# Performance work log

Hardware: AMD Instinct MI355X
Metric: run time of the kernel (lower is better)

Reference implementation:

```python
import jax, jax.numpy as jnp
import numpy as np

NUM_GRAPHS = 128
NODES_PER_GRAPH = 512
N_NODES = NUM_GRAPHS * NODES_PER_GRAPH
N_EDGES = 524288
IN_DIM = 128
HID = 128
OUT_DIM = 10
N_LAYERS = 3
POOL_RATIO = 0.5  # TopKPooling default ratio


def setup_inputs() -> dict:
    key = jax.random.key(0)
    ks = jax.random.split(key, 16)
    x = jax.random.normal(ks[0], (N_NODES, IN_DIM), dtype=jnp.float32)
    edge_index = jax.random.randint(ks[1], (2, N_EDGES), 0, N_NODES, dtype=jnp.int64)
    batch = jnp.repeat(jnp.arange(NUM_GRAPHS, dtype=jnp.int64), NODES_PER_GRAPH)
    s = 0.05
    return {
        "x": x,
        "edge_index": edge_index,
        "batch": batch,
        "emb_W": jax.random.normal(ks[2], (IN_DIM, HID), dtype=jnp.float32) * s,
        "emb_b": jnp.zeros((HID,), dtype=jnp.float32),
        "gcn_W": jax.random.normal(ks[3], (N_LAYERS, HID, HID), dtype=jnp.float32) * s,
        "gcn_b": jnp.zeros((N_LAYERS, HID), dtype=jnp.float32),
        "pool_p": jax.random.normal(ks[4], (HID,), dtype=jnp.float32),
        "fc1_W": jax.random.normal(ks[5], (HID, 128), dtype=jnp.float32) * s,
        "fc1_b": jnp.zeros((128,), dtype=jnp.float32),
        "fc2_W": jax.random.normal(ks[6], (128, 64), dtype=jnp.float32) * s,
        "fc2_b": jnp.zeros((64,), dtype=jnp.float32),
        "fc3_W": jax.random.normal(ks[7], (64, OUT_DIM), dtype=jnp.float32) * s,
        "fc3_b": jnp.zeros((OUT_DIM,), dtype=jnp.float32),
    }


def reference(x, edge_index, batch, emb_W, emb_b, gcn_W, gcn_b, pool_p,
              fc1_W, fc1_b, fc2_W, fc2_b, fc3_W, fc3_b):
    n = x.shape[0]
    # embedding
    h = x @ emb_W + emb_b
    # GCNConv normalization (PyG semantics): add self loops, deg from target scatter
    loop = jnp.arange(n, dtype=edge_index.dtype)
    src = jnp.concatenate([edge_index[0], loop])
    dst = jnp.concatenate([edge_index[1], loop])
    deg = jax.ops.segment_sum(jnp.ones_like(src, dtype=h.dtype), dst, num_segments=n)
    dinv = jnp.where(deg > 0, jax.lax.rsqrt(jnp.maximum(deg, 1e-12)), 0.0)
    norm = dinv[src] * dinv[dst]  # [E+n]
    for l in range(gcn_W.shape[0]):
        hw = h @ gcn_W[l]                                   # [n, HID]
        msg = hw[src] * norm[:, None]                        # gather + scale
        h = jax.nn.relu(jax.ops.segment_sum(msg, dst, num_segments=n) + gcn_b[l])
    # TopKPooling (ratio=0.5, tanh nonlinearity), uniform graphs -> reshape + top_k
    npg = n // NUM_GRAPHS
    k = int(np.ceil(POOL_RATIO * npg))
    score = (h @ pool_p) / jnp.linalg.norm(pool_p)           # [n]
    score_g = score.reshape(NUM_GRAPHS, npg)
    topv, topi = jax.lax.top_k(score_g, k)                   # [G, k]
    h_g = h.reshape(NUM_GRAPHS, npg, -1)
    h_sel = jnp.take_along_axis(h_g, topi[:, :, None], axis=1) * jnp.tanh(topv)[:, :, None]
    pooled = h_sel.mean(axis=1)                              # global_mean_pool -> [G, HID]
    # MLP head (dropout is identity in eval)
    z = jax.nn.relu(pooled @ fc1_W + fc1_b)
    z = jax.nn.relu(z @ fc2_W + fc2_b)
    return z @ fc3_W + fc3_b
```

## Files before the change

kernel.cpp:

```cpp
#include <hip/hip_runtime.h>
#include <hip/hip_bf16.h>
#include <math.h>


#define SLOTS 48

static __device__ __forceinline__ float4 f4add(float4 a, float4 b) {
    return make_float4(a.x + b.x, a.y + b.y, a.z + b.z, a.w + b.w);
}
static __device__ __forceinline__ float4 f4fma(float s, float4 a, float4 acc) {
    return make_float4(fmaf(s, a.x, acc.x), fmaf(s, a.y, acc.y),
                       fmaf(s, a.z, acc.z), fmaf(s, a.w, acc.w));
}

__global__ __launch_bounds__(256) void build_graph_fold(
    const int* __restrict__ src, const int* __restrict__ dst,
    int* __restrict__ cnt, int* __restrict__ csr_pad, int E, int EB,
    const float* __restrict__ embW, const float* __restrict__ embb,
    const float* __restrict__ W0, float* __restrict__ W01,
    float* __restrict__ b01, float* __restrict__ zrowA,
    float* __restrict__ zrowB)
{
    const int b = blockIdx.x;
    if (b < EB) {
        int e = b * 256 + threadIdx.x;
        if (e < E) {
            int d = dst[e];
            int r = atomicAdd(&cnt[d], 1);
            if (r < SLOTS) csr_pad[d * SLOTS + r] = src[e];
        }
        return;
    }
    __shared__ float rs[128];
    __shared__ float part[256];
    const int r = b - EB;
    const int t = threadIdx.x;
    if (r == 0 && t < 128) { zrowA[t] = 0.f; zrowB[t] = 0.f; }
    const int c = t & 127, q = t >> 7;
    if (t < 128) rs[t] = (r < 128) ? embW[r * 128 + t] : embb[t];
    __syncthreads();
    float s = 0.f;
    const int k0 = q * 64;
#pragma unroll 8
    for (int k = k0; k < k0 + 64; k++) s = fmaf(rs[k], W0[k * 128 + c], s);
    part[t] = s;
    __syncthreads();
    if (q == 0) {
        float v = part[c] + part[c + 128];
        if (r < 128) W01[r * 128 + c] = v;
        else         b01[c] = v;
    }
}

#define ASTRIDE 129
#define WSTRIDE 140
__global__ __launch_bounds__(256) void gemm128(
    const float* __restrict__ A, const float* __restrict__ W,
    const float* __restrict__ bias, const int* __restrict__ rowdeg,
    float* __restrict__ out, int n)
{
    __shared__ float As[32 * ASTRIDE];
    __shared__ float Ws[32 * WSTRIDE];
    const int tid  = threadIdx.x;
    const int rb   = blockIdx.x * 128;
    const int tc   = tid & 15;
    const int tr   = tid >> 4;
    const int colg = tc * 8;
    const int cswz = colg + ((colg >> 5) << 2);
    const int rowg = tr * 8;

    const int a_kq = tid & 7;
    const int a_m  = tid >> 3;
    const int w_c  = (tid & 31) * 4;
    const int w_cs = w_c + ((w_c >> 5) << 2);
    const int w_k  = tid >> 5;

    float acc[8][8];
#pragma unroll
    for (int i = 0; i < 8; i++)
#pragma unroll
        for (int j = 0; j < 8; j++) acc[i][j] = 0.f;

    float4 areg[4], wreg[4];
#pragma unroll
    for (int t = 0; t < 4; t++)
        areg[t] = *(const float4*)&A[(size_t)(rb + t * 32 + a_m) * 128 + a_kq * 4];
#pragma unroll
    for (int t = 0; t < 4; t++)
        wreg[t] = *(const float4*)&W[(size_t)(t * 8 + w_k) * 128 + w_c];

#pragma unroll 1
    for (int k0 = 0; k0 < 128; k0 += 32) {
#pragma unroll
        for (int t = 0; t < 4; t++) {
            const int m = t * 32 + a_m;
            const float4 av = areg[t];
            As[(a_kq * 4 + 0) * ASTRIDE + m] = av.x;
            As[(a_kq * 4 + 1) * ASTRIDE + m] = av.y;
            As[(a_kq * 4 + 2) * ASTRIDE + m] = av.z;
            As[(a_kq * 4 + 3) * ASTRIDE + m] = av.w;
        }
#pragma unroll
        for (int t = 0; t < 4; t++)
            *(float4*)&Ws[(t * 8 + w_k) * WSTRIDE + w_cs] = wreg[t];
        __syncthreads();
        if (k0 < 96) {
#pragma unroll
            for (int t = 0; t < 4; t++)
                areg[t] = *(const float4*)&A[(size_t)(rb + t * 32 + a_m) * 128 + k0 + 32 + a_kq * 4];
#pragma unroll
            for (int t = 0; t < 4; t++)
                wreg[t] = *(const float4*)&W[(size_t)(k0 + 32 + t * 8 + w_k) * 128 + w_c];
        }
#pragma unroll 8
        for (int kk = 0; kk < 32; kk++) {
            float4 a0 = *(const float4*)&As[kk * ASTRIDE + rowg];
            float4 a1 = *(const float4*)&As[kk * ASTRIDE + rowg + 4];
            float4 b0 = *(const float4*)&Ws[kk * WSTRIDE + cswz];
            float4 b1 = *(const float4*)&Ws[kk * WSTRIDE + cswz + 4];
            float av[8] = {a0.x, a0.y, a0.z, a0.w, a1.x, a1.y, a1.z, a1.w};
            float bv[8] = {b0.x, b0.y, b0.z, b0.w, b1.x, b1.y, b1.z, b1.w};
#pragma unroll
            for (int i = 0; i < 8; i++)
#pragma unroll
                for (int j = 0; j < 8; j++) acc[i][j] = fmaf(av[i], bv[j], acc[i][j]);
        }
        __syncthreads();
    }

    float4 bb0 = make_float4(0.f, 0.f, 0.f, 0.f), bb1 = bb0;
    if (bias) {
        bb0 = *(const float4*)&bias[colg];
        bb1 = *(const float4*)&bias[colg + 4];
    }
#pragma unroll
    for (int i = 0; i < 8; i++) {
        const int row  = rb + rowg + i;
        const float sc = rowdeg ? rsqrtf((float)(rowdeg[row] + 1)) : 1.f;
        float4 o0, o1;
        o0.x = (acc[i][0] + bb0.x) * sc;  o0.y = (acc[i][1] + bb0.y) * sc;
        o0.z = (acc[i][2] + bb0.z) * sc;  o0.w = (acc[i][3] + bb0.w) * sc;
        o1.x = (acc[i][4] + bb1.x) * sc;  o1.y = (acc[i][5] + bb1.y) * sc;
        o1.z = (acc[i][6] + bb1.z) * sc;  o1.w = (acc[i][7] + bb1.w) * sc;
        *(float4*)&out[(size_t)row * 128 + colg]     = o0;
        *(float4*)&out[(size_t)row * 128 + colg + 4] = o1;
    }
}

__global__ __launch_bounds__(256) void agg_gemm(
    const float* __restrict__ hs_in, const int* __restrict__ csr_pad,
    const int* __restrict__ cnt, const float* __restrict__ aggb,
    const float* __restrict__ W, float* __restrict__ hs_out, int n)
{
    __shared__ int   s_idx[128 * 17];
    __shared__ float s_dinv[128];
    __shared__ int   s_deg[128];
    __shared__ float As[32 * ASTRIDE];
    __shared__ float Ws[32 * WSTRIDE];

    const int tid = threadIdx.x;
    const int rb  = blockIdx.x * 128;
    const float4* __restrict__ hv = (const float4*)hs_in;

    if (tid < 128) {
        int d = cnt[rb + tid];
        s_deg[tid]  = d;
        s_dinv[tid] = rsqrtf((float)(d + 1));
    }
    {
        const int m    = tid >> 1;
        const int hf   = (tid & 1) * 8;
        const int node = rb + m;
        const int4 cA = *(const int4*)&csr_pad[node * SLOTS + hf];
        const int4 cB = *(const int4*)&csr_pad[node * SLOTS + hf + 4];
        const int  d  = cnt[node];
        int* row = &s_idx[m * 17 + hf];
        row[0] = (hf + 0 < d) ? cA.x : n;
        row[1] = (hf + 1 < d) ? cA.y : n;
        row[2] = (hf + 2 < d) ? cA.z : n;
        row[3] = (hf + 3 < d) ? cA.w : n;
        row[4] = (hf + 4 < d) ? cB.x : n;
        row[5] = (hf + 5 < d) ? cB.y : n;
        row[6] = (hf + 6 < d) ? cB.z : n;
        row[7] = (hf + 7 < d) ? cB.w : n;
    }
    __syncthreads();

    const int tc   = tid & 15;
    const int tr   = tid >> 4;
    const int colg = tc * 8;
    const int cswz = colg + ((colg >> 5) << 2);
    const int rowg = tr * 8;
    const int w_c  = (tid & 31) * 4;
    const int w_cs = w_c + ((w_c >> 5) << 2);
    const int w_k  = tid >> 5;
    const int ln = tid & 7;
    const int nd = tid >> 3;

    float acc[8][8];
#pragma unroll
    for (int i = 0; i < 8; i++)
#pragma unroll
        for (int j = 0; j < 8; j++) acc[i][j] = 0.f;

#pragma unroll 1
    for (int p = 0; p < 4; p++) {
        float4 wreg[4];
#pragma unroll
        for (int t = 0; t < 4; t++)
            wreg[t] = *(const float4*)&W[(size_t)(p * 32 + t * 8 + w_k) * 128 + w_c];

        const int fo = p * 8 + ln;
        const float4 bb = *(const float4*)&aggb[p * 32 + ln * 4];
#pragma unroll 1
        for (int ps = 0; ps < 4; ps++) {
            const int m    = ps * 32 + nd;
            const int node = rb + m;
            const int* rowI = &s_idx[m * 17];
            float4 self = hv[(size_t)node * 32 + fo];
            float4 r[16];
#pragma unroll
            for (int j = 0; j < 16; j++)
                r[j] = hv[(size_t)rowI[j] * 32 + fo];
            asm volatile("" ::: "memory");
            float4 a0 = self;
            float4 a1 = make_float4(0.f, 0.f, 0.f, 0.f);
            float4 a2 = a1, a3 = a1;
#pragma unroll
            for (int j = 0; j < 16; j += 4) {
                a0 = f4add(a0, r[j + 0]);
                a1 = f4add(a1, r[j + 1]);
                a2 = f4add(a2, r[j + 2]);
                a3 = f4add(a3, r[j + 3]);
            }
            const int d    = s_deg[m];
            const int dcap = d < SLOTS ? d : SLOTS;
            for (int j = 16; j < dcap; j++)
                a1 = f4add(a1, hv[(size_t)csr_pad[node * SLOTS + j] * 32 + fo]);
            float4 s = f4add(f4add(a0, a1), f4add(a2, a3));
            const float dv = s_dinv[m];
            float4 o;
            o.x = fmaxf(fmaf(s.x, dv, bb.x), 0.f);
            o.y = fmaxf(fmaf(s.y, dv, bb.y), 0.f);
            o.z = fmaxf(fmaf(s.z, dv, bb.z), 0.f);
            o.w = fmaxf(fmaf(s.w, dv, bb.w), 0.f);
            const int kb = ln * 4;
            As[(kb + 0) * ASTRIDE + m] = o.x;
            As[(kb + 1) * ASTRIDE + m] = o.y;
            As[(kb + 2) * ASTRIDE + m] = o.z;
            As[(kb + 3) * ASTRIDE + m] = o.w;
        }
#pragma unroll
        for (int t = 0; t < 4; t++)
            *(float4*)&Ws[(t * 8 + w_k) * WSTRIDE + w_cs] = wreg[t];
        __syncthreads();

#pragma unroll 8
        for (int kk = 0; kk < 32; kk++) {
            float4 a0 = *(const float4*)&As[kk * ASTRIDE + rowg];
            float4 a1 = *(const float4*)&As[kk * ASTRIDE + rowg + 4];
            float4 b0 = *(const float4*)&Ws[kk * WSTRIDE + cswz];
            float4 b1 = *(const float4*)&Ws[kk * WSTRIDE + cswz + 4];
            float av[8] = {a0.x, a0.y, a0.z, a0.w, a1.x, a1.y, a1.z, a1.w};
            float bv[8] = {b0.x, b0.y, b0.z, b0.w, b1.x, b1.y, b1.z, b1.w};
#pragma unroll
            for (int i = 0; i < 8; i++)
#pragma unroll
                for (int j = 0; j < 8; j++) acc[i][j] = fmaf(av[i], bv[j], acc[i][j]);
        }
        __syncthreads();
    }

#pragma unroll
    for (int i = 0; i < 8; i++) {
        const int row  = rb + rowg + i;
        const float sc = s_dinv[rowg + i];
        float4 o0, o1;
        o0.x = acc[i][0] * sc;  o0.y = acc[i][1] * sc;
        o0.z = acc[i][2] * sc;  o0.w = acc[i][3] * sc;
        o1.x = acc[i][4] * sc;  o1.y = acc[i][5] * sc;
        o1.z = acc[i][6] * sc;  o1.w = acc[i][7] * sc;
        *(float4*)&hs_out[(size_t)row * 128 + colg]     = o0;
        *(float4*)&hs_out[(size_t)row * 128 + colg + 4] = o1;
    }
}

__global__ __launch_bounds__(256) void aggregate(
    const float* __restrict__ hs, const int* __restrict__ csr_pad,
    const int* __restrict__ cnt, const float* __restrict__ bias,
    float* __restrict__ hout,
    const float* __restrict__ pool_p, float* __restrict__ scores, int n)
{
    const int grp  = threadIdx.x >> 5;
    const int lane = threadIdx.x & 31;
    const int node = blockIdx.x * 8 + grp;
    const float4* __restrict__ hv = (const float4*)hs;

    const int deg = cnt[node];
    const int e0  = node * SLOTS;

    int4 c4[4];
#pragma unroll
    for (int q = 0; q < 4; q++)
        c4[q] = *(const int4*)&csr_pad[e0 + q * 4];
    int ix[16] = {c4[0].x, c4[0].y, c4[0].z, c4[0].w,
                  c4[1].x, c4[1].y, c4[1].z, c4[1].w,
                  c4[2].x, c4[2].y, c4[2].z, c4[2].w,
                  c4[3].x, c4[3].y, c4[3].z, c4[3].w};
#pragma unroll
    for (int j = 0; j < 16; j++)
        ix[j] = (j < deg) ? ix[j] : n;

    float4 self = hv[(size_t)node * 32 + lane];
    float4 r[16];
#pragma unroll
    for (int j = 0; j < 16; j++)
        r[j] = hv[(size_t)ix[j] * 32 + lane];
    asm volatile("" ::: "memory");

    float4 a0 = self;
    float4 a1 = make_float4(0.f, 0.f, 0.f, 0.f);
    float4 a2 = a1, a3 = a1;
#pragma unroll
    for (int j = 0; j < 16; j += 4) {
        a0 = f4add(a0, r[j + 0]);
        a1 = f4add(a1, r[j + 1]);
        a2 = f4add(a2, r[j + 2]);
        a3 = f4add(a3, r[j + 3]);
    }
    const int dcap = deg < SLOTS ? deg : SLOTS;
    for (int j = 16; j < dcap; j++) {
        a1 = f4add(a1, hv[(size_t)csr_pad[e0 + j] * 32 + lane]);
    }

    float4 s = f4add(f4add(a0, a1), f4add(a2, a3));
    const float dv = rsqrtf((float)(deg + 1));
    const float4 bb = ((const float4*)bias)[lane];
    float4 o;
    o.x = fmaxf(fmaf(s.x, dv, bb.x), 0.f);
    o.y = fmaxf(fmaf(s.y, dv, bb.y), 0.f);
    o.z = fmaxf(fmaf(s.z, dv, bb.z), 0.f);
    o.w = fmaxf(fmaf(s.w, dv, bb.w), 0.f);
    ((float4*)hout)[(size_t)node * 32 + lane] = o;

    if (scores) {
        float4 pv = ((const float4*)pool_p)[lane];
        float d  = o.x * pv.x + o.y * pv.y + o.z * pv.z + o.w * pv.w;
        float nn = pv.x * pv.x + pv.y * pv.y + pv.z * pv.z + pv.w * pv.w;
#pragma unroll
        for (int off = 16; off > 0; off >>= 1) {
            d  += __shfl_xor(d, off);
            nn += __shfl_xor(nn, off);
        }
        if (lane == 0) scores[node] = d * rsqrtf(nn);
    }
}

__global__ __launch_bounds__(512) void topk_mlp(
    const float* __restrict__ scores, const float* __restrict__ h,
    const float* __restrict__ fc1W, const float* __restrict__ fc1b,
    const float* __restrict__ fc2W, const float* __restrict__ fc2b,
    const float* __restrict__ fc3W, const float* __restrict__ fc3b,
    float* __restrict__ out)
{
    __shared__ float s[512];
    __shared__ int   sel[256];
    __shared__ float w[256];
    __shared__ float4 red[512];
    __shared__ float pld[128];
    __shared__ float z1[128];
    __shared__ float z2[64];
    const int g = blockIdx.x;
    const int i = threadIdx.x;
    s[i] = scores[g * 512 + i];
    __syncthreads();
    float si = s[i];
    int rank = 0;
    for (int j = 0; j < 512; j++) {
        float sj = s[j];
        rank += (sj > si) || (sj == si && j < i);
    }
    if (rank < 256) {
        sel[rank] = i;
        w[rank]   = tanhf(si) * (1.f / 256.f);
    }
    __syncthreads();
    const int c   = (i & 31) * 4;
    const int grp = i >> 5;
    float4 acc = make_float4(0.f, 0.f, 0.f, 0.f);
    for (int t = grp; t < 256; t += 16) {
        float wt  = w[t];
        int   idx = sel[t];
        float4 r = *(const float4*)&h[((size_t)g * 512 + idx) * 128 + c];
        acc = f4fma(wt, r, acc);
    }
    red[i] = acc;
    __syncthreads();
    if (i < 256) red[i] = f4add(red[i], red[i + 256]);
    __syncthreads();
    if (i < 128) red[i] = f4add(red[i], red[i + 128]);
    __syncthreads();
    if (i < 64) red[i] = f4add(red[i], red[i + 64]);
    __syncthreads();
    if (i < 32) {
        float4 v = f4add(red[i], red[i + 32]);
        *(float4*)&pld[i * 4] = v;
    }
    __syncthreads();
    if (i < 128) {
        float a = fc1b[i];
        for (int k = 0; k < 128; k++) a += pld[k] * fc1W[k * 128 + i];
        z1[i] = fmaxf(a, 0.f);
    }
    __syncthreads();
    if (i < 64) {
        float b = fc2b[i];
        for (int k = 0; k < 128; k++) b += z1[k] * fc2W[k * 64 + i];
        z2[i] = fmaxf(b, 0.f);
    }
    __syncthreads();
    if (i < 10) {
        float o = fc3b[i];
        for (int k = 0; k < 64; k++) o += z2[k] * fc3W[k * 10 + i];
        out[g * 10 + i] = o;
    }
}

extern "C" void kernel_launch(void* const* d_in, const int* in_sizes, int n_in,
                              void* d_out, int out_size, void* d_ws, size_t ws_size,
                              hipStream_t stream)
{
    const float* x     = (const float*)d_in[0];
    const int*   eidx  = (const int*)d_in[1];
    const float* embW  = (const float*)d_in[3];
    const float* embb  = (const float*)d_in[4];
    const float* gcnW  = (const float*)d_in[5];
    const float* gcnb  = (const float*)d_in[6];
    const float* poolp = (const float*)d_in[7];
    const float* fc1W  = (const float*)d_in[8];
    const float* fc1b  = (const float*)d_in[9];
    const float* fc2W  = (const float*)d_in[10];
    const float* fc2b  = (const float*)d_in[11];
    const float* fc3W  = (const float*)d_in[12];
    const float* fc3b  = (const float*)d_in[13];
    float* out = (float*)d_out;

    const int n = in_sizes[0] / 128;
    const int E = in_sizes[1] / 2;
    const int G = n / 512;

    const int* src = eidx;
    const int* dst = eidx + E;

    char* ws = (char*)d_ws;
    size_t off = 0;
    auto carve = [&](size_t bytes) {
        void* p = ws + off;
        off += (bytes + 255) & ~(size_t)255;
        return p;
    };
    float* h       = (float*)carve((size_t)n * 128 * 4);
    float* hsA     = (float*)carve((size_t)(n + 1) * 128 * 4);
    float* hsB     = (float*)carve((size_t)(n + 1) * 128 * 4);
    int*   cnt     = (int*)carve((size_t)n * 4);
    int*   csr_pad = (int*)carve((size_t)n * SLOTS * 4);
    float* scores  = (float*)carve((size_t)n * 4);
    float* W01     = (float*)carve(128 * 128 * 4);
    float* b01     = (float*)carve(128 * 4);
    (void)ws_size;

    const int EB = E / 256;

    hipMemsetAsync(cnt, 0, (size_t)n * 4, stream);
    build_graph_fold<<<EB + 129, 256, 0, stream>>>(
        src, dst, cnt, csr_pad, E, EB, embW, embb, gcnW, W01, b01,
        hsA + (size_t)n * 128, hsB + (size_t)n * 128);

    gemm128<<<n / 128, 256, 0, stream>>>(x, W01, b01, cnt, hsA, n);

    agg_gemm<<<n / 128, 256, 0, stream>>>(hsA, csr_pad, cnt, gcnb,
                                          gcnW + (size_t)1 * 128 * 128, hsB, n);
    agg_gemm<<<n / 128, 256, 0, stream>>>(hsB, csr_pad, cnt, gcnb + 128,
                                          gcnW + (size_t)2 * 128 * 128, hsA, n);

    aggregate<<<n / 8, 256, 0, stream>>>(hsA, csr_pad, cnt, gcnb + 256, h,
                                         poolp, scores, n);

    topk_mlp<<<G, 512, 0, stream>>>(scores, h, fc1W, fc1b, fc2W, fc2b,
                                    fc3W, fc3b, out);
}
```

Measured before the change: 353.5 us.

## Fuse top-k pooling and MLP into final aggregation via last-block-per-graph atomics

The final aggregation kernel now counts finished blocks per graph with an atomic counter. The last of the 64 blocks covering a graph then performs the top-k selection, weighted pooling and MLP head in place, so the separate topk_mlp launch is removed. The counters sit in the memset cnt region. agg_gemm also gets a min-blocks-per-CU hint of 2, which may constrain its registers. The tail work now runs on only 128 blocks of 256 threads, each ranking two scores per thread, and correctness depends on threadfence ordering.

```diff
diff --git a/kernel.cpp b/kernel.cpp
--- a/kernel.cpp
+++ b/kernel.cpp
@@ -147,7 +147,7 @@
     }
 }
 
-__global__ __launch_bounds__(256) void agg_gemm(
+__global__ __launch_bounds__(256, 2) void agg_gemm(
     const float* __restrict__ hs_in, const int* __restrict__ csr_pad,
     const int* __restrict__ cnt, const float* __restrict__ aggb,
     const float* __restrict__ W, float* __restrict__ hs_out, int n)
@@ -285,11 +285,16 @@
     }
 }
 
-__global__ __launch_bounds__(256) void aggregate(
+__global__ __launch_bounds__(256) void aggregate_topk(
     const float* __restrict__ hs, const int* __restrict__ csr_pad,
     const int* __restrict__ cnt, const float* __restrict__ bias,
     float* __restrict__ hout,
-    const float* __restrict__ pool_p, float* __restrict__ scores, int n)
+    const float* __restrict__ pool_p, float* __restrict__ scores,
+    int* __restrict__ gdone,
+    const float* __restrict__ fc1W, const float* __restrict__ fc1b,
+    const float* __restrict__ fc2W, const float* __restrict__ fc2b,
+    const float* __restrict__ fc3W, const float* __restrict__ fc3b,
+    float* __restrict__ out, int n)
 {
     const int grp  = threadIdx.x >> 5;
     const int lane = threadIdx.x & 31;
@@ -343,7 +348,7 @@
     o.w = fmaxf(fmaf(s.w, dv, bb.w), 0.f);
     ((float4*)hout)[(size_t)node * 32 + lane] = o;
 
-    if (scores) {
+    {
         float4 pv = ((const float4*)pool_p)[lane];
         float d  = o.x * pv.x + o.y * pv.y + o.z * pv.z + o.w * pv.w;
         float nn = pv.x * pv.x + pv.y * pv.y + pv.z * pv.z + pv.w * pv.w;
@@ -354,49 +359,50 @@
         }
         if (lane == 0) scores[node] = d * rsqrtf(nn);
     }
-}
-
-__global__ __launch_bounds__(512) void topk_mlp(
-    const float* __restrict__ scores, const float* __restrict__ h,
-    const float* __restrict__ fc1W, const float* __restrict__ fc1b,
-    const float* __restrict__ fc2W, const float* __restrict__ fc2b,
-    const float* __restrict__ fc3W, const float* __restrict__ fc3b,
-    float* __restrict__ out)
-{
-    __shared__ float s[512];
+
+    __shared__ int is_last;
+    const int g = blockIdx.x >> 6;
+    __syncthreads();
+    if (threadIdx.x == 0) {
+        __threadfence();
+        int prev = atomicAdd(&gdone[g], 1);
+        is_last = (prev == 63);
+        if (prev == 63) __threadfence();
+    }
+    __syncthreads();
+    if (!is_last) return;
+
+    __shared__ float sc[512];
     __shared__ int   sel[256];
     __shared__ float w[256];
-    __shared__ float4 red[512];
+    __shared__ float4 red[256];
     __shared__ float pld[128];
     __shared__ float z1[128];
     __shared__ float z2[64];
-    const int g = blockIdx.x;
     const int i = threadIdx.x;
-    s[i] = scores[g * 512 + i];
-    __syncthreads();
-    float si = s[i];
-    int rank = 0;
+    sc[i]       = scores[g * 512 + i];
+    sc[i + 256] = scores[g * 512 + i + 256];
+    __syncthreads();
+    const float sa = sc[i], sb = sc[i + 256];
+    int ra = 0, rb2 = 0;
     for (int j = 0; j < 512; j++) {
-        float sj = s[j];
-        rank += (sj > si) || (sj == si && j < i);
-    }
-    if (rank < 256) {
-        sel[rank] = i;
-        w[rank]   = tanhf(si) * (1.f / 256.f);
-    }
-    __syncthreads();
-    const int c   = (i & 31) * 4;
-    const int grp = i >> 5;
+        const float sj = sc[j];
+        ra  += (sj > sa) || (sj == sa && j < i);
+        rb2 += (sj > sb) || (sj == sb && j < i + 256);
+    }
+    if (ra < 256)  { sel[ra]  = i;       w[ra]  = tanhf(sa) * (1.f / 256.f); }
+    if (rb2 < 256) { sel[rb2] = i + 256; w[rb2] = tanhf(sb) * (1.f / 256.f); }
+    __syncthreads();
+    const int c  = (i & 31) * 4;
+    const int gq = i >> 5;
     float4 acc = make_float4(0.f, 0.f, 0.f, 0.f);
-    for (int t = grp; t < 256; t += 16) {
+    for (int t = gq; t < 256; t += 8) {
         float wt  = w[t];
         int   idx = sel[t];
-        float4 r = *(const float4*)&h[((size_t)g * 512 + idx) * 128 + c];
-        acc = f4fma(wt, r, acc);
+        float4 hr = *(const float4*)&hout[((size_t)g * 512 + idx) * 128 + c];
+        acc = f4fma(wt, hr, acc);
     }
     red[i] = acc;
-    __syncthreads();
-    if (i < 256) red[i] = f4add(red[i], red[i + 256]);
     __syncthreads();
     if (i < 128) red[i] = f4add(red[i], red[i + 128]);
     __syncthreads();
@@ -420,9 +426,9 @@
     }
     __syncthreads();
     if (i < 10) {
-        float o = fc3b[i];
-        for (int k = 0; k < 64; k++) o += z2[k] * fc3W[k * 10 + i];
-        out[g * 10 + i] = o;
+        float oo = fc3b[i];
+        for (int k = 0; k < 64; k++) oo += z2[k] * fc3W[k * 10 + i];
+        out[g * 10 + i] = oo;
     }
 }
 
@@ -462,16 +468,18 @@
     float* h       = (float*)carve((size_t)n * 128 * 4);
     float* hsA     = (float*)carve((size_t)(n + 1) * 128 * 4);
     float* hsB     = (float*)carve((size_t)(n + 1) * 128 * 4);
-    int*   cnt     = (int*)carve((size_t)n * 4);
+    int*   cnt     = (int*)carve((size_t)(n + G) * 4);
     int*   csr_pad = (int*)carve((size_t)n * SLOTS * 4);
     float* scores  = (float*)carve((size_t)n * 4);
     float* W01     = (float*)carve(128 * 128 * 4);
     float* b01     = (float*)carve(128 * 4);
     (void)ws_size;
 
+    int* gdone = cnt + n;
+
     const int EB = E / 256;
 
-    hipMemsetAsync(cnt, 0, (size_t)n * 4, stream);
+    hipMemsetAsync(cnt, 0, (size_t)(n + G) * 4, stream);
     build_graph_fold<<<EB + 129, 256, 0, stream>>>(
         src, dst, cnt, csr_pad, E, EB, embW, embb, gcnW, W01, b01,
         hsA + (size_t)n * 128, hsB + (size_t)n * 128);
@@ -483,9 +491,7 @@
     agg_gemm<<<n / 128, 256, 0, stream>>>(hsB, csr_pad, cnt, gcnb + 128,
                                           gcnW + (size_t)2 * 128 * 128, hsA, n);
 
-    aggregate<<<n / 8, 256, 0, stream>>>(hsA, csr_pad, cnt, gcnb + 256, h,
-                                         poolp, scores, n);
-
-    topk_mlp<<<G, 512, 0, stream>>>(scores, h, fc1W, fc1b, fc2W, fc2b,
-                                    fc3W, fc3b, out);
-}
+    aggregate_topk<<<n / 8, 256, 0, stream>>>(
+        hsA, csr_pad, cnt, gcnb + 256, h, poolp, scores, gdone,
+        fc1W, fc1b, fc2W, fc2b, fc3W, fc3b, out, n);
+}
```

After: 663.1 us. 87.6% more time.
